# Performance work log

Measured on AMD Instinct MI355X. Metric: run time of the kernel, lower is better.

Reference implementation:

```python
import jax, jax.numpy as jnp
import numpy as np
import math

HIDDEN = 2048
N_Q = 16
N_KV = 8
HEAD_DIM = 128
THETA = 10000.0
RANK = 8
ALPHA = 16
LORA_SCALING = ALPHA / RANK  # 2.0
SCALING = 1.0 / math.sqrt(HEAD_DIM)


def setup_inputs() -> dict:
    key = jax.random.key(0)
    ks = jax.random.split(key, 14)
    B, S = 2, 2048
    std = 0.02
    inp = {
        "x": jax.random.normal(ks[0], (B, S, HIDDEN), dtype=jnp.float32),
        # nn.Linear weights: [out_features, in_features]
        "Wq": jax.random.normal(ks[1], (N_Q * HEAD_DIM, HIDDEN), dtype=jnp.float32) * std,
        "Wk": jax.random.normal(ks[2], (N_KV * HEAD_DIM, HIDDEN), dtype=jnp.float32) * std,
        "Wv": jax.random.normal(ks[3], (N_KV * HEAD_DIM, HIDDEN), dtype=jnp.float32) * std,
        "Wo": jax.random.normal(ks[4], (HIDDEN, N_Q * HEAD_DIM), dtype=jnp.float32) * std,
        "qA": jax.random.normal(ks[5], (RANK, HIDDEN), dtype=jnp.float32) * std,
        "qB": jax.random.normal(ks[6], (N_Q * HEAD_DIM, RANK), dtype=jnp.float32) * std,
        "kA": jax.random.normal(ks[7], (RANK, HIDDEN), dtype=jnp.float32) * std,
        "kB": jax.random.normal(ks[8], (N_KV * HEAD_DIM, RANK), dtype=jnp.float32) * std,
        "vA": jax.random.normal(ks[9], (RANK, HIDDEN), dtype=jnp.float32) * std,
        "vB": jax.random.normal(ks[10], (N_KV * HEAD_DIM, RANK), dtype=jnp.float32) * std,
        "oA": jax.random.normal(ks[11], (RANK, N_Q * HEAD_DIM), dtype=jnp.float32) * std,
        "oB": jax.random.normal(ks[12], (HIDDEN, RANK), dtype=jnp.float32) * std,
    }
    return inp


def _rope_cos_sin(seq_len, dtype):
    inv_freq = 1.0 / (THETA ** (jnp.arange(0, HEAD_DIM, 2, dtype=jnp.float32) / HEAD_DIM))
    t = jnp.arange(seq_len, dtype=jnp.float32)
    freqs = t[:, None] * inv_freq[None, :]  # [S, D/2]
    return jnp.cos(freqs).astype(dtype), jnp.sin(freqs).astype(dtype)


def _apply_rope(x, cos, sin):
    # x: [B, H, S, D]; interleaved real/imag pairs on last dim
    xr = x[..., ::2]
    xi = x[..., 1::2]
    rr = xr * cos - xi * sin
    ri = xr * sin + xi * cos
    return jnp.stack([rr, ri], axis=-1).reshape(x.shape)


def _forward(x, Wq, Wk, Wv, Wo, qA, qB, kA, kB, vA, vB, oA, oB):
    B, S, H = x.shape
    # base projections + LoRA (low-rank path kept factored: (x @ A^T) @ B^T)
    q = x @ Wq.T + ((x @ qA.T) @ qB.T) * LORA_SCALING  # [B,S,NQ*D]
    k = x @ Wk.T + ((x @ kA.T) @ kB.T) * LORA_SCALING  # [B,S,NKV*D]
    v = x @ Wv.T + ((x @ vA.T) @ vB.T) * LORA_SCALING
    q = q.reshape(B, S, N_Q, HEAD_DIM).transpose(0, 2, 1, 3)   # [B,NQ,S,D]
    k = k.reshape(B, S, N_KV, HEAD_DIM).transpose(0, 2, 1, 3)  # [B,NKV,S,D]
    v = v.reshape(B, S, N_KV, HEAD_DIM).transpose(0, 2, 1, 3)
    cos, sin = _rope_cos_sin(S, x.dtype)  # [S, D/2] each
    q = _apply_rope(q, cos, sin)
    k = _apply_rope(k, cos, sin)
    if N_Q != N_KV:
        rep = N_Q // N_KV
        k = jnp.repeat(k, rep, axis=1)  # [B,NQ,S,D]
        v = jnp.repeat(v, rep, axis=1)
    scores = jnp.einsum('bhqd,bhkd->bhqk', q, k) * SCALING
    causal = jnp.tril(jnp.ones((S, S), dtype=bool))
    scores = jnp.where(causal, scores, -jnp.inf)
    attn = jax.nn.softmax(scores, axis=-1).astype(v.dtype)
    out = jnp.einsum('bhqk,bhkd->bhqd', attn, v)  # [B,NQ,S,D]
    out = out.transpose(0, 2, 1, 3).reshape(B, S, N_Q * HEAD_DIM)
    return out @ Wo.T + ((out @ oA.T) @ oB.T) * LORA_SCALING


def reference(x, Wq, Wk, Wv, Wo, qA, qB, kA, kB, vA, vB, oA, oB):
    return _forward(x, Wq, Wk, Wv, Wo, qA, qB, kA, kB, vA, vB, oA, oB)
```

## Files before the change

kernel.cpp:

```cpp
#include <hip/hip_runtime.h>
#include <hip/hip_bf16.h>
#include <cmath>

#define HIDDEN 2048
#define SEQ 2048
#define BATCH 2
#define NQ 16
#define NKV 8
#define HD 128
#define RANKL 8
#define LORA_SCALE 2.0f
#define INV_SQRT_D 0.08838834764831845f
#define LOG2E 1.4426950408889634f
#define SM_SCALE (INV_SQRT_D * LOG2E)

typedef unsigned short ushort_t;
typedef __bf16 bf16x8 __attribute__((ext_vector_type(8)));
typedef float f32x4 __attribute__((ext_vector_type(4)));

static __device__ __forceinline__ ushort_t f2bf(float f) {
    __hip_bfloat16 h = __float2bfloat16(f);
    return *(ushort_t*)&h;
}
static __device__ __forceinline__ float bf2f(ushort_t u) {
    unsigned int v = ((unsigned int)u) << 16;
    return __builtin_bit_cast(float, v);
}
static __device__ __forceinline__ void gload_lds16(const ushort_t* g, ushort_t* l) {
    __builtin_amdgcn_global_load_lds(
        (const __attribute__((address_space(1))) unsigned int*)g,
        (__attribute__((address_space(3))) unsigned int*)l, 16, 0, 0);
}

__global__ __launch_bounds__(256) void prep_fused(
    const float* __restrict__ X, ushort_t* __restrict__ Xbf,
    const float* __restrict__ qA, const float* __restrict__ kA,
    const float* __restrict__ vA,
    float* __restrict__ oq, float* __restrict__ ok, float* __restrict__ ov,
    const float* __restrict__ Wq, const float* __restrict__ Wk,
    const float* __restrict__ Wv, const float* __restrict__ Wo,
    ushort_t* __restrict__ Wqb, ushort_t* __restrict__ Wkb,
    ushort_t* __restrict__ Wvb, ushort_t* __restrict__ Wob)
{
    __shared__ float wred[4][3][RANKL];
    int t = threadIdx.x;
    if (blockIdx.x < 4096) {
        int m = blockIdx.x;
        int c0 = t * 8;
        const float* xr = X + (size_t)m * HIDDEN + c0;
        float4 a = *(const float4*)xr;
        float4 b = *(const float4*)(xr + 4);
        float xv[8] = {a.x, a.y, a.z, a.w, b.x, b.y, b.z, b.w};
        uint4 o;
        o.x = (unsigned int)f2bf(xv[0]) | ((unsigned int)f2bf(xv[1]) << 16);
        o.y = (unsigned int)f2bf(xv[2]) | ((unsigned int)f2bf(xv[3]) << 16);
        o.z = (unsigned int)f2bf(xv[4]) | ((unsigned int)f2bf(xv[5]) << 16);
        o.w = (unsigned int)f2bf(xv[6]) | ((unsigned int)f2bf(xv[7]) << 16);
        *(uint4*)(Xbf + (size_t)m * HIDDEN + c0) = o;

        float p[3][RANKL];
#pragma unroll
        for (int w = 0; w < 3; w++)
#pragma unroll
            for (int r = 0; r < RANKL; r++) p[w][r] = 0.f;
        const float* Aw[3] = {qA, kA, vA};
#pragma unroll
        for (int e = 0; e < 8; e++) {
            float x8 = xv[e];
#pragma unroll
            for (int w = 0; w < 3; w++)
#pragma unroll
                for (int r = 0; r < RANKL; r++)
                    p[w][r] += x8 * Aw[w][r * HIDDEN + c0 + e];
        }
#pragma unroll
        for (int w = 0; w < 3; w++)
#pragma unroll
            for (int r = 0; r < RANKL; r++) {
                float v = p[w][r];
                v += __shfl_xor(v, 32); v += __shfl_xor(v, 16);
                v += __shfl_xor(v, 8);  v += __shfl_xor(v, 4);
                v += __shfl_xor(v, 2);  v += __shfl_xor(v, 1);
                p[w][r] = v;
            }
        int wave = t >> 6, lane = t & 63;
        if (lane == 0) {
#pragma unroll
            for (int w = 0; w < 3; w++)
#pragma unroll
                for (int r = 0; r < RANKL; r++) wred[wave][w][r] = p[w][r];
        }
        __syncthreads();
        if (t < 3 * RANKL) {
            int w = t / RANKL, r = t % RANKL;
            float s = wred[0][w][r] + wred[1][w][r] + wred[2][w][r] + wred[3][w][r];
            float* dst = (w == 0) ? oq : (w == 1) ? ok : ov;
            dst[(size_t)m * RANKL + r] = s;
        }
    } else {
        size_t i = (size_t)(blockIdx.x - 4096) * 256 + t;
        const float* src; ushort_t* dst; size_t j;
        if (i < 524288)       { src = Wq; dst = Wqb; j = i; }
        else if (i < 786432)  { src = Wk; dst = Wkb; j = i - 524288; }
        else if (i < 1048576) { src = Wv; dst = Wvb; j = i - 786432; }
        else                  { src = Wo; dst = Wob; j = i - 1048576; }
        const float4* p = (const float4*)src + j * 2;
        float4 a = p[0], b = p[1];
        uint4 o;
        o.x = (unsigned int)f2bf(a.x) | ((unsigned int)f2bf(a.y) << 16);
        o.y = (unsigned int)f2bf(a.z) | ((unsigned int)f2bf(a.w) << 16);
        o.z = (unsigned int)f2bf(b.x) | ((unsigned int)f2bf(b.y) << 16);
        o.w = (unsigned int)f2bf(b.z) | ((unsigned int)f2bf(b.w) << 16);
        *(uint4*)(dst + j * 8) = o;
    }
}

__global__ __launch_bounds__(256) void lora_xa_bf16(
    const ushort_t* __restrict__ X, const float* __restrict__ Aw,
    float* __restrict__ out, int K)
{
    int m = blockIdx.x;
    int t = threadIdx.x;
    const ushort_t* xr = X + (size_t)m * K;
    float p[RANKL];
#pragma unroll
    for (int r = 0; r < RANKL; r++) p[r] = 0.f;
    for (int c = t; c < K; c += 256) {
        float xv = bf2f(xr[c]);
#pragma unroll
        for (int r = 0; r < RANKL; r++) p[r] += xv * Aw[r * K + c];
    }
#pragma unroll
    for (int r = 0; r < RANKL; r++) {
        float v = p[r];
        v += __shfl_xor(v, 32); v += __shfl_xor(v, 16);
        v += __shfl_xor(v, 8);  v += __shfl_xor(v, 4);
        v += __shfl_xor(v, 2);  v += __shfl_xor(v, 1);
        p[r] = v;
    }
    __shared__ float wred[4][RANKL];
    int wave = t >> 6, lane = t & 63;
    if (lane == 0) {
#pragma unroll
        for (int r = 0; r < RANKL; r++) wred[wave][r] = p[r];
    }
    __syncthreads();
    if (t < RANKL) {
        out[(size_t)m * RANKL + t] =
            wred[0][t] + wred[1][t] + wred[2][t] + wred[3][t];
    }
}

static __device__ __forceinline__ void gemm_core(
    const ushort_t* __restrict__ A, const ushort_t* __restrict__ B,
    void* __restrict__ Cout, int N, int K, int bm, int bn,
    const float* __restrict__ xa, const float* __restrict__ LB,
    float lscale, int out_bf16, ushort_t* As, ushort_t* Bs)
{
    const int t = threadIdx.x;
    const int lane = t & 63;
    const int w = t >> 6;
    const int quad = lane >> 4;
    const int c = lane & 15;

    const int wm = (w & 1) * 64;
    const int wn = (w >> 1) * 64;

    f32x4 acc[4][4];
#pragma unroll
    for (int i = 0; i < 4; i++)
#pragma unroll
        for (int j = 0; j < 4; j++) acc[i][j] = (f32x4){0.f, 0.f, 0.f, 0.f};

    const int p0 = w * 64 + lane;
    const int p1 = 256 + w * 64 + lane;
    const int r0 = p0 >> 2, g0 = (p0 & 3) ^ ((p0 >> 3) & 3);
    const int r1 = p1 >> 2, g1 = (p1 & 3) ^ ((p1 >> 3) & 3);
    const ushort_t* gA0 = A + (size_t)(bm + r0) * K + g0 * 8;
    const ushort_t* gA1 = A + (size_t)(bm + r1) * K + g1 * 8;
    const ushort_t* gB0 = B + (size_t)(bn + r0) * K + g0 * 8;
    const ushort_t* gB1 = B + (size_t)(bn + r1) * K + g1 * 8;
    ushort_t* lA0 = As + (size_t)(w * 64) * 8;
    ushort_t* lA1 = As + (size_t)(256 + w * 64) * 8;
    ushort_t* lB0 = Bs + (size_t)(w * 64) * 8;
    ushort_t* lB1 = Bs + (size_t)(256 + w * 64) * 8;

    const int csw = quad ^ ((c >> 1) & 3);

    for (int k0 = 0; k0 < K; k0 += 32) {
        __syncthreads();
        gload_lds16(gA0 + k0, lA0);
        gload_lds16(gA1 + k0, lA1);
        gload_lds16(gB0 + k0, lB0);
        gload_lds16(gB1 + k0, lB1);
        __syncthreads();

        bf16x8 af[4], bfr[4];
#pragma unroll
        for (int mt = 0; mt < 4; mt++)
            af[mt] = *(const bf16x8*)&As[((wm + mt * 16 + c) * 4 + csw) * 8];
#pragma unroll
        for (int nt = 0; nt < 4; nt++)
            bfr[nt] = *(const bf16x8*)&Bs[((wn + nt * 16 + c) * 4 + csw) * 8];
#pragma unroll
        for (int mt = 0; mt < 4; mt++)
#pragma unroll
            for (int nt = 0; nt < 4; nt++)
                acc[mt][nt] = __builtin_amdgcn_mfma_f32_16x16x32_bf16(
                    af[mt], bfr[nt], acc[mt][nt], 0, 0, 0);
    }

    float lb[4][RANKL];
#pragma unroll
    for (int nt = 0; nt < 4; nt++) {
        int col = bn + wn + nt * 16 + c;
        float4 u = *(const float4*)&LB[(size_t)col * RANKL];
        float4 v = *(const float4*)&LB[(size_t)col * RANKL + 4];
        lb[nt][0] = u.x; lb[nt][1] = u.y; lb[nt][2] = u.z; lb[nt][3] = u.w;
        lb[nt][4] = v.x; lb[nt][5] = v.y; lb[nt][6] = v.z; lb[nt][7] = v.w;
    }
#pragma unroll
    for (int mt = 0; mt < 4; mt++) {
        float la[4][RANKL];
#pragma unroll
        for (int r = 0; r < 4; r++) {
            int row = bm + wm + mt * 16 + quad * 4 + r;
            float4 u = *(const float4*)&xa[(size_t)row * RANKL];
            float4 v = *(const float4*)&xa[(size_t)row * RANKL + 4];
            la[r][0] = u.x; la[r][1] = u.y; la[r][2] = u.z; la[r][3] = u.w;
            la[r][4] = v.x; la[r][5] = v.y; la[r][6] = v.z; la[r][7] = v.w;
        }
#pragma unroll
        for (int nt = 0; nt < 4; nt++) {
#pragma unroll
            for (int r = 0; r < 4; r++) {
                float s = 0.f;
#pragma unroll
                for (int k = 0; k < RANKL; k++) s += la[r][k] * lb[nt][k];
                float val = acc[mt][nt][r] + lscale * s;
                size_t row = bm + wm + mt * 16 + quad * 4 + r;
                size_t col = bn + wn + nt * 16 + c;
                if (out_bf16)
                    ((ushort_t*)Cout)[row * N + col] = f2bf(val);
                else
                    ((float*)Cout)[row * N + col] = val;
            }
        }
    }
}

#define BKT 64
#define NKT (HIDDEN / BKT)

__global__ __launch_bounds__(512, 2) void gemm_qkv256(
    const ushort_t* __restrict__ A,
    const ushort_t* __restrict__ Wqb, const ushort_t* __restrict__ Wkb,
    const ushort_t* __restrict__ Wvb,
    ushort_t* __restrict__ q_lin, ushort_t* __restrict__ k_lin,
    ushort_t* __restrict__ v_lin,
    const float* __restrict__ xa_q, const float* __restrict__ xa_k,
    const float* __restrict__ xa_v,
    const float* __restrict__ qB, const float* __restrict__ kB,
    const float* __restrict__ vB)
{
    __shared__ __align__(16) ushort_t As[2][256 * BKT];
    __shared__ __align__(16) ushort_t Bs[2][256 * BKT];

    const int t = threadIdx.x;
    const int lane = t & 63;
    const int w = t >> 6;
    const int wm = w >> 2;
    const int wn = w & 3;
    const int quad = lane >> 4;
    const int c = lane & 15;
    const int c7 = c & 7;

    const int bc = blockIdx.y;
    const ushort_t* Bmat; ushort_t* Cout; const float* xa; const float* LB;
    int N, bn;
    if (bc < 8)       { Bmat = Wqb; Cout = q_lin; xa = xa_q; LB = qB; N = 2048; bn = bc * 256; }
    else if (bc < 12) { Bmat = Wkb; Cout = k_lin; xa = xa_k; LB = kB; N = 1024; bn = (bc - 8) * 256; }
    else              { Bmat = Wvb; Cout = v_lin; xa = xa_v; LB = vB; N = 1024; bn = (bc - 12) * 256; }
    const int bm = blockIdx.x * 256;

    const int r8  = lane >> 3;
    const int ksl = (lane & 7) ^ r8;
    const int ga  = wn;
    const int bh  = wn >> 1;
    const int gb  = wm * 2 + (wn & 1);

    const ushort_t* gAb = A    + (size_t)(bm + wm * 128 + ga * 8 + r8) * HIDDEN + ksl * 8;
    const ushort_t* gBb = Bmat + (size_t)(bn + bh * 128 + gb * 8 + r8) * HIDDEN + ksl * 8;
    const int lAoff = (wm * 128 + ga * 8) * BKT;
    const int lBoff = (bh * 128 + gb * 8) * BKT;

#pragma unroll
    for (int j = 0; j < 4; j++) {
        gload_lds16(gAb + (size_t)j * 32 * HIDDEN, &As[0][lAoff + j * 32 * BKT]);
        gload_lds16(gBb + (size_t)j * 32 * HIDDEN, &Bs[0][lBoff + j * 32 * BKT]);
    }
#pragma unroll
    for (int j = 0; j < 3; j++) {
        gload_lds16(gAb + (size_t)j * 32 * HIDDEN + BKT, &As[1][lAoff + j * 32 * BKT]);
        gload_lds16(gBb + (size_t)j * 32 * HIDDEN + BKT, &Bs[1][lBoff + j * 32 * BKT]);
    }

    f32x4 acc[8][4];
#pragma unroll
    for (int i = 0; i < 8; i++)
#pragma unroll
        for (int j = 0; j < 4; j++) acc[i][j] = (f32x4){0.f, 0.f, 0.f, 0.f};

#pragma unroll 1
    for (int T = 0; T < NKT; ++T) {
        const int cur = T & 1;
        const ushort_t* cA = As[cur];
        const ushort_t* cB = Bs[cur];
        bf16x8 bfr[4][2];

#pragma unroll
        for (int q = 0; q < 4; ++q) {
            if (q == 0) {
                asm volatile("s_waitcnt vmcnt(6)" ::: "memory");
            }
            __builtin_amdgcn_sched_barrier(0);
            __builtin_amdgcn_s_barrier();
            __builtin_amdgcn_sched_barrier(0);

            bf16x8 af[2][2];
#pragma unroll
            for (int m2 = 0; m2 < 2; ++m2) {
                const int row = wm * 128 + (q * 2 + m2) * 16 + c;
#pragma unroll
                for (int kh = 0; kh < 2; ++kh)
                    af[m2][kh] = *(const bf16x8*)
                        &cA[row * BKT + (((kh * 4 + quad) ^ c7) * 8)];
            }
            if (q == 0) {
#pragma unroll
                for (int nt = 0; nt < 4; ++nt) {
                    const int rowb = wn * 64 + nt * 16 + c;
#pragma unroll
                    for (int kh = 0; kh < 2; ++kh)
                        bfr[nt][kh] = *(const bf16x8*)
                            &cB[rowb * BKT + (((kh * 4 + quad) ^ c7) * 8)];
                }
            }

            if (q == 0) {
                const int tl = T + 1;
                if (tl < NKT) {
                    gload_lds16(gAb + (size_t)3 * 32 * HIDDEN + (size_t)tl * BKT,
                                &As[cur ^ 1][lAoff + 3 * 32 * BKT]);
                    gload_lds16(gBb + (size_t)3 * 32 * HIDDEN + (size_t)tl * BKT,
                                &Bs[cur ^ 1][lBoff + 3 * 32 * BKT]);
                }
            } else {
                const int tl = T + 2;
                if (tl < NKT) {
                    const int j = q - 1;
                    gload_lds16(gAb + (size_t)j * 32 * HIDDEN + (size_t)tl * BKT,
                                &As[cur][lAoff + j * 32 * BKT]);
                    gload_lds16(gBb + (size_t)j * 32 * HIDDEN + (size_t)tl * BKT,
                                &Bs[cur][lBoff + j * 32 * BKT]);
                }
            }

            __builtin_amdgcn_s_setprio(1);
#pragma unroll
            for (int m2 = 0; m2 < 2; ++m2)
#pragma unroll
                for (int nt = 0; nt < 4; ++nt)
#pragma unroll
                    for (int kh = 0; kh < 2; ++kh)
                        acc[q * 2 + m2][nt] = __builtin_amdgcn_mfma_f32_16x16x32_bf16(
                            af[m2][kh], bfr[nt][kh], acc[q * 2 + m2][nt], 0, 0, 0);
            __builtin_amdgcn_s_setprio(0);
        }
    }

    float lb[4][RANKL];
#pragma unroll
    for (int nt = 0; nt < 4; nt++) {
        int col = bn + wn * 64 + nt * 16 + c;
        float4 u = *(const float4*)&LB[(size_t)col * RANKL];
        float4 v = *(const float4*)&LB[(size_t)col * RANKL + 4];
        lb[nt][0] = u.x; lb[nt][1] = u.y; lb[nt][2] = u.z; lb[nt][3] = u.w;
        lb[nt][4] = v.x; lb[nt][5] = v.y; lb[nt][6] = v.z; lb[nt][7] = v.w;
    }
#pragma unroll
    for (int mt = 0; mt < 8; mt++) {
        float la[4][RANKL];
#pragma unroll
        for (int r = 0; r < 4; r++) {
            int row = bm + wm * 128 + mt * 16 + quad * 4 + r;
            float4 u = *(const float4*)&xa[(size_t)row * RANKL];
            float4 v = *(const float4*)&xa[(size_t)row * RANKL + 4];
            la[r][0] = u.x; la[r][1] = u.y; la[r][2] = u.z; la[r][3] = u.w;
            la[r][4] = v.x; la[r][5] = v.y; la[r][6] = v.z; la[r][7] = v.w;
        }
#pragma unroll
        for (int nt = 0; nt < 4; nt++) {
#pragma unroll
            for (int r = 0; r < 4; r++) {
                float s = 0.f;
#pragma unroll
                for (int k = 0; k < RANKL; k++) s += la[r][k] * lb[nt][k];
                float val = acc[mt][nt][r] + LORA_SCALE * s;
                size_t row = bm + wm * 128 + mt * 16 + quad * 4 + r;
                size_t col = bn + wn * 64 + nt * 16 + c;
                Cout[row * N + col] = f2bf(val);
            }
        }
    }
}

__global__ __launch_bounds__(256) void gemm_wo(
    const ushort_t* __restrict__ A, const ushort_t* __restrict__ Wob,
    float* __restrict__ out, const float* __restrict__ xa_o,
    const float* __restrict__ oB)
{
    __shared__ ushort_t As[128 * 32];
    __shared__ ushort_t Bs[128 * 32];
    gemm_core(A, Wob, out, HIDDEN, NQ * HD, blockIdx.x * 128, blockIdx.y * 128,
              xa_o, oB, LORA_SCALE, 0, As, Bs);
}

__global__ __launch_bounds__(256) void reshape_fused(
    const ushort_t* __restrict__ qlin, const ushort_t* __restrict__ klin,
    ushort_t* __restrict__ qb, ushort_t* __restrict__ kb,
    const ushort_t* __restrict__ vlin, ushort_t* __restrict__ Vt)
{
    __shared__ ushort_t tile[64 * 72];
    int t = threadIdx.x;
    if (blockIdx.x < 4096) {
        int bs = blockIdx.x;
        int s = bs & (SEQ - 1);
        int b = bs >> 11;
        int p = t & 63;
        float inv = exp2f(-(float)p * 0.20762050593046f);
        float ang = (float)s * inv;
        float cc = cosf(ang), si = sinf(ang);
#pragma unroll
        for (int j = 0; j < 6; j++) {
            int item = t + 256 * j;
            int hh = item >> 6;
            unsigned int pk;
            ushort_t* dst;
            if (hh < NQ) {
                pk = *(const unsigned int*)&qlin[(size_t)bs * (NQ * HD) + hh * HD + 2 * p];
                dst = qb + (((size_t)(b * NQ + hh) * SEQ) + s) * HD + 2 * p;
            } else {
                int kh = hh - NQ;
                pk = *(const unsigned int*)&klin[(size_t)bs * (NKV * HD) + kh * HD + 2 * p];
                dst = kb + (((size_t)(b * NKV + kh) * SEQ) + s) * HD + 2 * p;
            }
            float xr = bf2f((ushort_t)(pk & 0xffff));
            float xi = bf2f((ushort_t)(pk >> 16));
            float rr = xr * cc - xi * si;
            float ri = xr * si + xi * cc;
            *(unsigned int*)dst = ((unsigned int)f2bf(ri) << 16) | f2bf(rr);
        }
    } else {
        int idx = blockIdx.x - 4096;
        int bk = idx >> 6;
        int rem = idx & 63;
        int b = bk >> 3, kvh = bk & 7;
        int s0 = (rem >> 1) * 64, d0 = (rem & 1) * 64;
#pragma unroll
        for (int i = 0; i < 2; i++) {
            int id = t + 256 * i;
            int r = id >> 3, cc = id & 7;
            uint4 v = *(const uint4*)&vlin[(size_t)(b * SEQ + s0 + r) * (NKV * HD)
                                           + kvh * HD + d0 + cc * 8];
            *(uint4*)&tile[r * 72 + cc * 8] = v;
        }
        __syncthreads();
#pragma unroll
        for (int i = 0; i < 2; i++) {
            int id = t + 256 * i;
            int dr = id >> 3, sc = id & 7;
            ushort_t tmp[8];
#pragma unroll
            for (int e = 0; e < 8; e++) tmp[e] = tile[(sc * 8 + e) * 72 + dr];
            *(uint4*)&Vt[((size_t)(b * NKV + kvh) * HD + d0 + dr) * SEQ + s0 + sc * 8]
                = *(uint4*)tmp;
        }
    }
}

__global__ __launch_bounds__(256, 2) void attn_mfma3(
    const ushort_t* __restrict__ Q, const ushort_t* __restrict__ K,
    const ushort_t* __restrict__ V, ushort_t* __restrict__ O)
{
    __shared__ ushort_t Ks[2][64 * 128];
    __shared__ ushort_t Vs[2][128 * 64];
    __shared__ ushort_t Psh[4][16 * 68];

    const int t = threadIdx.x;
    const int lane = t & 63;
    const int w = t >> 6;
    const int quad = lane >> 4;
    const int c = lane & 15;
    const int q4 = quad * 4;
    const int c7 = c & 7;

    const int head = blockIdx.x >> 4;
    const int a = blockIdx.x & 15;
    const int h = head & (NQ - 1);
    const int b = head >> 4;
    const int kvh = b * NKV + (h >> 1);

    const ushort_t* Kg = K + (size_t)kvh * SEQ * HD;
    const ushort_t* Vg = V + (size_t)kvh * HD * SEQ;

    const ushort_t* gK[4]; const ushort_t* gV[4];
    int lo[4];
#pragma unroll
    for (int i = 0; i < 4; i++) {
        int cid = t + 256 * i;
        int kr = cid >> 4, kc = cid & 15;
        gK[i] = Kg + (size_t)kr * HD + ((kc ^ (kr & 7)) * 8);
        int vd = cid >> 3, vc = cid & 7;
        gV[i] = Vg + (size_t)vd * SEQ + ((vc ^ (vd & 7)) * 8);
        lo[i] = (i * 256 + (t & ~63)) * 8;
    }

#pragma unroll 1
    for (int half = 0; half < 2; half++) {
        const int qt = half ? (31 - a) : a;
        const int qb0 = qt * 64;
        const int myrow = qb0 + w * 16;

        const ushort_t* Qg = Q + ((size_t)head * SEQ + myrow + c) * HD;
        bf16x8 qf[4];
#pragma unroll
        for (int ch = 0; ch < 4; ch++)
            qf[ch] = *(const bf16x8*)(Qg + ch * 32 + quad * 8);

        f32x4 o[8];
#pragma unroll
        for (int i = 0; i < 8; i++) o[i] = (f32x4){0.f, 0.f, 0.f, 0.f};
        float lp[4] = {0.f, 0.f, 0.f, 0.f};

        const int ntiles = qt + 1;

#pragma unroll
        for (int i = 0; i < 4; i++) gload_lds16(gK[i], &Ks[0][lo[i]]);
#pragma unroll
        for (int i = 0; i < 4; i++) gload_lds16(gV[i], &Vs[0][lo[i]]);
        __syncthreads();

        for (int tile = 0; tile < ntiles; ++tile) {
            const int cur = tile & 1;
            if (tile + 1 < ntiles) {
                const int j1 = (tile + 1) * 64;
#pragma unroll
                for (int i = 0; i < 4; i++)
                    gload_lds16(gK[i] + (size_t)j1 * HD, &Ks[cur ^ 1][lo[i]]);
#pragma unroll
                for (int i = 0; i < 4; i++)
                    gload_lds16(gV[i] + j1, &Vs[cur ^ 1][lo[i]]);
            }

            f32x4 s[4];
#pragma unroll
            for (int tt = 0; tt < 4; tt++) s[tt] = (f32x4){0.f, 0.f, 0.f, 0.f};
#pragma unroll
            for (int tt = 0; tt < 4; tt++) {
                const int krow = tt * 16 + c;
#pragma unroll
                for (int ch = 0; ch < 4; ch++) {
                    bf16x8 kf = *(const bf16x8*)
                        &Ks[cur][krow * 128 + (((ch * 4 + quad) ^ c7) * 8)];
                    s[tt] = __builtin_amdgcn_mfma_f32_16x16x32_bf16(
                        qf[ch], kf, s[tt], 0, 0, 0);
                }
            }

            const bool diag = (tile == qt);
            const int j0 = tile * 64;
#pragma unroll
            for (int r = 0; r < 4; r++) {
                const int row_g = myrow + q4 + r;
#pragma unroll
                for (int tt = 0; tt < 4; tt++) {
                    float p = exp2f(s[tt][r] * SM_SCALE);
                    if (diag && (j0 + tt * 16 + c > row_g)) p = 0.f;
                    Psh[w][(q4 + r) * 68 + tt * 16 + c] = f2bf(p);
                    lp[r] += p;
                }
            }

            bf16x8 pf[2];
#pragma unroll
            for (int ch = 0; ch < 2; ch++) {
                int base = c * 68 + ch * 32 + quad * 8;
                uint2 aa = *(const uint2*)&Psh[w][base];
                uint2 bb = *(const uint2*)&Psh[w][base + 4];
                uint4 u; u.x = aa.x; u.y = aa.y; u.z = bb.x; u.w = bb.y;
                pf[ch] = __builtin_bit_cast(bf16x8, u);
            }

#pragma unroll
            for (int dt = 0; dt < 8; dt++) {
                const int vrow = dt * 16 + c;
#pragma unroll
                for (int ch = 0; ch < 2; ch++) {
                    bf16x8 vf = *(const bf16x8*)
                        &Vs[cur][vrow * 64 + (((ch * 4 + quad) ^ c7) * 8)];
                    o[dt] = __builtin_amdgcn_mfma_f32_16x16x32_bf16(
                        pf[ch], vf, o[dt], 0, 0, 0);
                }
            }
            __syncthreads();
        }

        float inv[4];
#pragma unroll
        for (int r = 0; r < 4; r++) {
            float v = lp[r];
            v += __shfl_xor(v, 1);
            v += __shfl_xor(v, 2);
            v += __shfl_xor(v, 4);
            v += __shfl_xor(v, 8);
            inv[r] = 1.f / v;
        }
        size_t base = ((size_t)b * SEQ + myrow + q4) * (NQ * HD) + h * HD + c;
#pragma unroll
        for (int r = 0; r < 4; r++)
#pragma unroll
            for (int dt = 0; dt < 8; dt++)
                O[base + (size_t)r * (NQ * HD) + dt * 16] =
                    f2bf(o[dt][r] * inv[r]);
    }
}

extern "C" void kernel_launch(void* const* d_in, const int* in_sizes, int n_in,
                              void* d_out, int out_size, void* d_ws, size_t ws_size,
                              hipStream_t stream)
{
    const float* x  = (const float*)d_in[0];
    const float* Wq = (const float*)d_in[1];
    const float* Wk = (const float*)d_in[2];
    const float* Wv = (const float*)d_in[3];
    const float* Wo = (const float*)d_in[4];
    const float* qA = (const float*)d_in[5];
    const float* qB = (const float*)d_in[6];
    const float* kA = (const float*)d_in[7];
    const float* kB = (const float*)d_in[8];
    const float* vA = (const float*)d_in[9];
    const float* vB = (const float*)d_in[10];
    const float* oA = (const float*)d_in[11];
    const float* oB = (const float*)d_in[12];
    float* out = (float*)d_out;
    float* ws = (float*)d_ws;

    const int M = BATCH * SEQ;

    float* xa_q = ws;
    float* xa_k = ws + 32768;
    float* xa_v = ws + 65536;
    float* xa_o = ws + 98304;
    ushort_t* q_lin = (ushort_t*)(ws + 131072);
    ushort_t* k_lin = (ushort_t*)(ws + 4325376);
    ushort_t* v_lin = (ushort_t*)(ws + 6422528);
    ushort_t* qb    = (ushort_t*)(ws + 8519680);
    ushort_t* kb    = (ushort_t*)(ws + 12713984);
    ushort_t* vtb   = (ushort_t*)(ws + 14811136);
    ushort_t* xbf   = (ushort_t*)(ws + 16908288);
    ushort_t* Wqb   = (ushort_t*)(ws + 21102592);
    ushort_t* Wkb   = (ushort_t*)(ws + 23199744);
    ushort_t* Wvb   = (ushort_t*)(ws + 24248320);
    ushort_t* Wob   = (ushort_t*)(ws + 25296896);
    ushort_t* attn_out = q_lin;

    prep_fused<<<4096 + 6144, 256, 0, stream>>>(
        x, xbf, qA, kA, vA, xa_q, xa_k, xa_v,
        Wq, Wk, Wv, Wo, Wqb, Wkb, Wvb, Wob);

    gemm_qkv256<<<dim3(M / 256, 16), 512, 0, stream>>>(
        xbf, Wqb, Wkb, Wvb, q_lin, k_lin, v_lin,
        xa_q, xa_k, xa_v, qB, kB, vB);

    reshape_fused<<<4096 + 1024, 256, 0, stream>>>(
        q_lin, k_lin, qb, kb, v_lin, vtb);

    attn_mfma3<<<512, 256, 0, stream>>>(qb, kb, vtb, attn_out);

    lora_xa_bf16<<<M, 256, 0, stream>>>(attn_out, oA, xa_o, NQ * HD);
    gemm_wo<<<dim3(M / 128, HIDDEN / 128), 256, 0, stream>>>(
        attn_out, Wob, out, xa_o, oB);
}
```

Baseline: 389.2 us.

## Compute LoRA down-projections with MFMA blocks over 16-row tiles

Moves the x·A^T LoRA down-projections for q/k/v out of the per-row cast blocks into separate blocks of the prep kernel. Each of these blocks handles 16 rows with bf16 MFMA 16x16x32, splitting K across four waves and reducing the partial sums through LDS. The o-projection LoRA reduction is rewritten the same way, launching 256 blocks instead of one per row. This cuts scalar FMA work and the shuffle reductions. In exchange, the fp32 x and A operands are rounded to bf16 before multiplying, which adds some numerical error, and part of each MFMA is padded with zeros.

```diff
diff --git a/kernel.cpp b/kernel.cpp
--- a/kernel.cpp
+++ b/kernel.cpp
@@ -31,74 +31,43 @@
         (const __attribute__((address_space(1))) unsigned int*)g,
         (__attribute__((address_space(3))) unsigned int*)l, 16, 0, 0);
 }
+static __device__ __forceinline__ bf16x8 pack8(float4 a, float4 b) {
+    uint4 u;
+    u.x = (unsigned int)f2bf(a.x) | ((unsigned int)f2bf(a.y) << 16);
+    u.y = (unsigned int)f2bf(a.z) | ((unsigned int)f2bf(a.w) << 16);
+    u.z = (unsigned int)f2bf(b.x) | ((unsigned int)f2bf(b.y) << 16);
+    u.w = (unsigned int)f2bf(b.z) | ((unsigned int)f2bf(b.w) << 16);
+    return __builtin_bit_cast(bf16x8, u);
+}
 
 __global__ __launch_bounds__(256) void prep_fused(
     const float* __restrict__ X, ushort_t* __restrict__ Xbf,
     const float* __restrict__ qA, const float* __restrict__ kA,
     const float* __restrict__ vA,
-    float* __restrict__ oq, float* __restrict__ ok, float* __restrict__ ov,
+    float* __restrict__ xa_q, float* __restrict__ xa_k,
+    float* __restrict__ xa_v,
     const float* __restrict__ Wq, const float* __restrict__ Wk,
     const float* __restrict__ Wv, const float* __restrict__ Wo,
     ushort_t* __restrict__ Wqb, ushort_t* __restrict__ Wkb,
     ushort_t* __restrict__ Wvb, ushort_t* __restrict__ Wob)
 {
-    __shared__ float wred[4][3][RANKL];
-    int t = threadIdx.x;
-    if (blockIdx.x < 4096) {
-        int m = blockIdx.x;
+    __shared__ f32x4 red[4][2][64];
+    const int t = threadIdx.x;
+    const int bid = blockIdx.x;
+
+    if (bid < 4096) {
         int c0 = t * 8;
-        const float* xr = X + (size_t)m * HIDDEN + c0;
+        const float* xr = X + (size_t)bid * HIDDEN + c0;
         float4 a = *(const float4*)xr;
         float4 b = *(const float4*)(xr + 4);
-        float xv[8] = {a.x, a.y, a.z, a.w, b.x, b.y, b.z, b.w};
         uint4 o;
-        o.x = (unsigned int)f2bf(xv[0]) | ((unsigned int)f2bf(xv[1]) << 16);
-        o.y = (unsigned int)f2bf(xv[2]) | ((unsigned int)f2bf(xv[3]) << 16);
-        o.z = (unsigned int)f2bf(xv[4]) | ((unsigned int)f2bf(xv[5]) << 16);
-        o.w = (unsigned int)f2bf(xv[6]) | ((unsigned int)f2bf(xv[7]) << 16);
-        *(uint4*)(Xbf + (size_t)m * HIDDEN + c0) = o;
-
-        float p[3][RANKL];
-#pragma unroll
-        for (int w = 0; w < 3; w++)
-#pragma unroll
-            for (int r = 0; r < RANKL; r++) p[w][r] = 0.f;
-        const float* Aw[3] = {qA, kA, vA};
-#pragma unroll
-        for (int e = 0; e < 8; e++) {
-            float x8 = xv[e];
-#pragma unroll
-            for (int w = 0; w < 3; w++)
-#pragma unroll
-                for (int r = 0; r < RANKL; r++)
-                    p[w][r] += x8 * Aw[w][r * HIDDEN + c0 + e];
-        }
-#pragma unroll
-        for (int w = 0; w < 3; w++)
-#pragma unroll
-            for (int r = 0; r < RANKL; r++) {
-                float v = p[w][r];
-                v += __shfl_xor(v, 32); v += __shfl_xor(v, 16);
-                v += __shfl_xor(v, 8);  v += __shfl_xor(v, 4);
-                v += __shfl_xor(v, 2);  v += __shfl_xor(v, 1);
-                p[w][r] = v;
-            }
-        int wave = t >> 6, lane = t & 63;
-        if (lane == 0) {
-#pragma unroll
-            for (int w = 0; w < 3; w++)
-#pragma unroll
-                for (int r = 0; r < RANKL; r++) wred[wave][w][r] = p[w][r];
-        }
-        __syncthreads();
-        if (t < 3 * RANKL) {
-            int w = t / RANKL, r = t % RANKL;
-            float s = wred[0][w][r] + wred[1][w][r] + wred[2][w][r] + wred[3][w][r];
-            float* dst = (w == 0) ? oq : (w == 1) ? ok : ov;
-            dst[(size_t)m * RANKL + r] = s;
-        }
-    } else {
-        size_t i = (size_t)(blockIdx.x - 4096) * 256 + t;
+        o.x = (unsigned int)f2bf(a.x) | ((unsigned int)f2bf(a.y) << 16);
+        o.y = (unsigned int)f2bf(a.z) | ((unsigned int)f2bf(a.w) << 16);
+        o.z = (unsigned int)f2bf(b.x) | ((unsigned int)f2bf(b.y) << 16);
+        o.w = (unsigned int)f2bf(b.z) | ((unsigned int)f2bf(b.w) << 16);
+        *(uint4*)(Xbf + (size_t)bid * HIDDEN + c0) = o;
+    } else if (bid < 10240) {
+        size_t i = (size_t)(bid - 4096) * 256 + t;
         const float* src; ushort_t* dst; size_t j;
         if (i < 524288)       { src = Wq; dst = Wqb; j = i; }
         else if (i < 786432)  { src = Wk; dst = Wkb; j = i - 524288; }
@@ -112,42 +81,106 @@
         o.z = (unsigned int)f2bf(b.x) | ((unsigned int)f2bf(b.y) << 16);
         o.w = (unsigned int)f2bf(b.z) | ((unsigned int)f2bf(b.w) << 16);
         *(uint4*)(dst + j * 8) = o;
-    }
-}
-
-__global__ __launch_bounds__(256) void lora_xa_bf16(
-    const ushort_t* __restrict__ X, const float* __restrict__ Aw,
-    float* __restrict__ out, int K)
+    } else {
+        const int m0 = (bid - 10240) * 16;
+        const int lane = t & 63;
+        const int w = t >> 6;
+        const int c = lane & 15;
+        const int quad = lane >> 4;
+
+        const float* b0 = (c < 8) ? (qA + (size_t)c * HIDDEN)
+                                  : (kA + (size_t)(c - 8) * HIDDEN);
+        const float* b1 = vA + (size_t)(c & 7) * HIDDEN;
+        const bool b1v = (c < 8);
+        const float* ax = X + (size_t)(m0 + c) * HIDDEN;
+
+        f32x4 acc0 = (f32x4){0.f, 0.f, 0.f, 0.f};
+        f32x4 acc1 = (f32x4){0.f, 0.f, 0.f, 0.f};
+        const int kbase = w * 512 + quad * 8;
+#pragma unroll
+        for (int ks = 0; ks < 16; ++ks) {
+            const int k = kbase + ks * 32;
+            float4 x0 = *(const float4*)&ax[k];
+            float4 x1 = *(const float4*)&ax[k + 4];
+            float4 p0a = *(const float4*)&b0[k];
+            float4 p0b = *(const float4*)&b0[k + 4];
+            float4 p1a = {0.f, 0.f, 0.f, 0.f}, p1b = {0.f, 0.f, 0.f, 0.f};
+            if (b1v) { p1a = *(const float4*)&b1[k]; p1b = *(const float4*)&b1[k + 4]; }
+            bf16x8 af = pack8(x0, x1);
+            bf16x8 bf0 = pack8(p0a, p0b);
+            bf16x8 bf1 = pack8(p1a, p1b);
+            acc0 = __builtin_amdgcn_mfma_f32_16x16x32_bf16(af, bf0, acc0, 0, 0, 0);
+            acc1 = __builtin_amdgcn_mfma_f32_16x16x32_bf16(af, bf1, acc1, 0, 0, 0);
+        }
+        red[w][0][lane] = acc0;
+        red[w][1][lane] = acc1;
+        __syncthreads();
+        if (t < 64) {
+#pragma unroll
+            for (int nt = 0; nt < 2; ++nt) {
+                f32x4 s = red[0][nt][t];
+#pragma unroll
+                for (int ww = 1; ww < 4; ++ww) {
+                    f32x4 o = red[ww][nt][t];
+                    s[0] += o[0]; s[1] += o[1]; s[2] += o[2]; s[3] += o[3];
+                }
+                int col = nt * 16 + (t & 15);
+                if (col < 24) {
+                    float* dst = (col < 8) ? xa_q : (col < 16) ? xa_k : xa_v;
+                    int cc = col & 7;
+                    int row0 = m0 + (t >> 4) * 4;
+#pragma unroll
+                    for (int r = 0; r < 4; ++r)
+                        dst[(size_t)(row0 + r) * RANKL + cc] = s[r];
+                }
+            }
+        }
+    }
+}
+
+__global__ __launch_bounds__(256) void lora_o_mfma(
+    const ushort_t* __restrict__ Xo, const float* __restrict__ oA,
+    float* __restrict__ xa_o)
 {
-    int m = blockIdx.x;
-    int t = threadIdx.x;
-    const ushort_t* xr = X + (size_t)m * K;
-    float p[RANKL];
-#pragma unroll
-    for (int r = 0; r < RANKL; r++) p[r] = 0.f;
-    for (int c = t; c < K; c += 256) {
-        float xv = bf2f(xr[c]);
-#pragma unroll
-        for (int r = 0; r < RANKL; r++) p[r] += xv * Aw[r * K + c];
-    }
-#pragma unroll
-    for (int r = 0; r < RANKL; r++) {
-        float v = p[r];
-        v += __shfl_xor(v, 32); v += __shfl_xor(v, 16);
-        v += __shfl_xor(v, 8);  v += __shfl_xor(v, 4);
-        v += __shfl_xor(v, 2);  v += __shfl_xor(v, 1);
-        p[r] = v;
-    }
-    __shared__ float wred[4][RANKL];
-    int wave = t >> 6, lane = t & 63;
-    if (lane == 0) {
-#pragma unroll
-        for (int r = 0; r < RANKL; r++) wred[wave][r] = p[r];
-    }
+    __shared__ f32x4 red[4][64];
+    const int t = threadIdx.x;
+    const int lane = t & 63;
+    const int w = t >> 6;
+    const int c = lane & 15;
+    const int quad = lane >> 4;
+    const int m0 = blockIdx.x * 16;
+
+    const ushort_t* ax = Xo + (size_t)(m0 + c) * (NQ * HD);
+    const float* b0 = oA + (size_t)(c & 7) * (NQ * HD);
+    const bool bv = (c < 8);
+
+    f32x4 acc = (f32x4){0.f, 0.f, 0.f, 0.f};
+    const int kbase = w * 512 + quad * 8;
+#pragma unroll
+    for (int ks = 0; ks < 16; ++ks) {
+        const int k = kbase + ks * 32;
+        bf16x8 af = *(const bf16x8*)&ax[k];
+        float4 pa = {0.f, 0.f, 0.f, 0.f}, pb = {0.f, 0.f, 0.f, 0.f};
+        if (bv) { pa = *(const float4*)&b0[k]; pb = *(const float4*)&b0[k + 4]; }
+        bf16x8 bf = pack8(pa, pb);
+        acc = __builtin_amdgcn_mfma_f32_16x16x32_bf16(af, bf, acc, 0, 0, 0);
+    }
+    red[w][lane] = acc;
     __syncthreads();
-    if (t < RANKL) {
-        out[(size_t)m * RANKL + t] =
-            wred[0][t] + wred[1][t] + wred[2][t] + wred[3][t];
+    if (t < 64) {
+        f32x4 s = red[0][t];
+#pragma unroll
+        for (int ww = 1; ww < 4; ++ww) {
+            f32x4 o = red[ww][t];
+            s[0] += o[0]; s[1] += o[1]; s[2] += o[2]; s[3] += o[3];
+        }
+        int col = t & 15;
+        if (col < 8) {
+            int row0 = m0 + (t >> 4) * 4;
+#pragma unroll
+            for (int r = 0; r < 4; ++r)
+                xa_o[(size_t)(row0 + r) * RANKL + col] = s[r];
+        }
     }
 }
 
@@ -675,7 +708,7 @@
     ushort_t* Wob   = (ushort_t*)(ws + 25296896);
     ushort_t* attn_out = q_lin;
 
-    prep_fused<<<4096 + 6144, 256, 0, stream>>>(
+    prep_fused<<<4096 + 6144 + 256, 256, 0, stream>>>(
         x, xbf, qA, kA, vA, xa_q, xa_k, xa_v,
         Wq, Wk, Wv, Wo, Wqb, Wkb, Wvb, Wob);
 
@@ -688,7 +721,7 @@
 
     attn_mfma3<<<512, 256, 0, stream>>>(qb, kb, vtb, attn_out);
 
-    lora_xa_bf16<<<M, 256, 0, stream>>>(attn_out, oA, xa_o, NQ * HD);
+    lora_o_mfma<<<256, 256, 0, stream>>>(attn_out, oA, xa_o);
     gemm_wo<<<dim3(M / 128, HIDDEN / 128), 256, 0, stream>>>(
         attn_out, Wob, out, xa_o, oB);
 }
```

Result: faster. 371.8 us (-4.5%).
